# Kernel optimization log

Measured on AMD Instinct MI355X. Metric: run time of the kernel, lower is better.

Reference implementation:

```python
import jax, jax.numpy as jnp
import numpy as np

T, B, I, H = 512, 64, 300, 1000


def setup_inputs() -> dict:
    key = jax.random.key(0)
    k_in, k_wih, k_whh = jax.random.split(key, 3)
    s_ih = 1.0 / np.sqrt(H)
    return {
        "inputs": jax.random.normal(k_in, (T, B, I), dtype=jnp.float32),
        "h0": jnp.zeros((B, H), dtype=jnp.float32),
        "c0": jnp.zeros((B, H), dtype=jnp.float32),
        "W_ih": jax.random.normal(k_wih, (4 * H, I), dtype=jnp.float32) * s_ih,
        "W_hh": jax.random.normal(k_whh, (4 * H, H), dtype=jnp.float32) * s_ih,
        "b_ih": jnp.zeros((4 * H,), dtype=jnp.float32),
        "b_hh": jnp.zeros((4 * H,), dtype=jnp.float32),
    }


def reference(inputs, h0, c0, W_ih, W_hh, b_ih, b_hh):
    # Precompute input projections for all timesteps in one big GEMM:
    # [T,B,I] @ [I,4H] -> [T,B,4H]
    x_gates = jnp.einsum('tbi,gi->tbg', inputs, W_ih) + b_ih + b_hh

    def step(carry, xg):
        h, c = carry
        gates = xg + h @ W_hh.T            # [B, 4H]
        i, f, g, o = jnp.split(gates, 4, axis=-1)  # PyTorch gate order i,f,g,o
        i = jax.nn.sigmoid(i)
        f = jax.nn.sigmoid(f)
        g = jnp.tanh(g)
        o = jax.nn.sigmoid(o)
        c_new = f * c + i * g
        h_new = o * jnp.tanh(c_new)
        return (h_new, c_new), h_new

    (_, _), outputs = jax.lax.scan(step, (h0, c0), x_gates)
    return outputs  # [T, B, H] — stacked per-timestep outputs
```

## Files before the change

### kernel.cpp

```cpp
#include <hip/hip_runtime.h>

#define Tn 512
#define Bn 64
#define In 300
#define Hn 1000
#define G4H 4000
#define KP 1024
#define KI 320
#define NB 125

typedef __attribute__((ext_vector_type(8))) short bf16x8;
typedef __attribute__((ext_vector_type(4))) float f32x4;
typedef unsigned int u32;
typedef unsigned short u16;
typedef unsigned long long u64;

__device__ __forceinline__ u16 f2bf(float x) {
  union { float f; u32 u; } v; v.f = x;
  u32 r = (v.u + 0x7fffu + ((v.u >> 16) & 1u)) >> 16;
  return (u16)r;
}
__device__ __forceinline__ float bf2f(u16 s) {
  union { u32 u; float f; } v; v.u = ((u32)s) << 16;
  return v.f;
}
__device__ __forceinline__ float sigm(float x) { return 1.f / (1.f + __expf(-x)); }
__device__ __forceinline__ float tanh_f(float x) {
  float e = __expf(2.f * x);
  return 1.f - 2.f / (e + 1.f);
}

__device__ __forceinline__ u64 aload64(const u64* p) {
  return __hip_atomic_load((u64*)p, __ATOMIC_RELAXED, __HIP_MEMORY_SCOPE_AGENT);
}
__device__ __forceinline__ void astore64(u64* p, u64 v) {
  __hip_atomic_store(p, v, __ATOMIC_RELAXED, __HIP_MEMORY_SCOPE_AGENT);
}
__device__ __forceinline__ u32 aload32(const u32* p) {
  return __hip_atomic_load((u32*)p, __ATOMIC_RELAXED, __HIP_MEMORY_SCOPE_AGENT);
}
__device__ __forceinline__ void astore32(u32* p, u32 v) {
  __hip_atomic_store(p, v, __ATOMIC_RELAXED, __HIP_MEMORY_SCOPE_AGENT);
}

__global__ void conv_pad(const float* __restrict__ src, u16* __restrict__ dst,
                         int rows, int scols, int dcols) {
  int idx = blockIdx.x * 256 + threadIdx.x;
  int total = rows * dcols;
  if (idx >= total) return;
  int r = idx / dcols, k = idx - r * dcols;
  float v = (k < scols) ? src[(size_t)r * scols + k] : 0.f;
  dst[idx] = f2bf(v);
}

__global__ void init_scan(const float* __restrict__ h0, u16* __restrict__ ring,
                          u32* __restrict__ bar) {
  int idx = blockIdx.x * 256 + threadIdx.x;
  if (idx < 4096) bar[idx] = 0;
  if (idx < Bn * KP) {
    int b = idx >> 10, k = idx & (KP - 1);
    float v = (k < Hn) ? h0[b * Hn + k] : 0.f;
    ring[idx] = f2bf(v);
  }
  for (int i = idx; i < (Tn - 1) * Bn * 24; i += 512 * 256) {
    int slot = 1 + i / (Bn * 24);
    int rem = i % (Bn * 24);
    int row = rem / 24, col = 1000 + (rem % 24);
    ring[(size_t)slot * (Bn * KP) + (size_t)row * KP + col] = 0;
  }
}

template<bool XF32>
__global__ void __launch_bounds__(256)
gemm_xg(const u16* __restrict__ A, const u16* __restrict__ Wb,
        const float* __restrict__ b_ih, const float* __restrict__ b_hh,
        void* __restrict__ xg_out) {
  const int lane = threadIdx.x & 63, w = threadIdx.x >> 6;
  const int m0 = blockIdx.x * 64, n0 = blockIdx.y * 64;
  f32x4 acc[4] = {};
  const int arow = m0 + w * 16 + (lane & 15);
  const int koff = (lane >> 4) * 8;
  int nrow[4];
#pragma unroll
  for (int nt = 0; nt < 4; ++nt) {
    int n = n0 + nt * 16 + (lane & 15);
    nrow[nt] = (n < G4H) ? n : (G4H - 1);
  }
  for (int kc = 0; kc < KI / 32; ++kc) {
    bf16x8 a = *(const bf16x8*)(A + (size_t)arow * KI + kc * 32 + koff);
#pragma unroll
    for (int nt = 0; nt < 4; ++nt) {
      bf16x8 bb = *(const bf16x8*)(Wb + (size_t)nrow[nt] * KI + kc * 32 + koff);
      acc[nt] = __builtin_amdgcn_mfma_f32_16x16x32_bf16(a, bb, acc[nt], 0, 0, 0);
    }
  }
#pragma unroll
  for (int nt = 0; nt < 4; ++nt) {
    int col = n0 + nt * 16 + (lane & 15);
    if (col >= G4H) continue;
    float bias = b_ih[col] + b_hh[col];
    u32 g = (u32)col / 1000u;
    int j = col - (int)g * 1000;
    int nb8 = j >> 3, cc = j & 7;
    int slot = ((int)g << 3) | cc;
    int mrow = m0 + w * 16 + (lane >> 4) * 4;
#pragma unroll
    for (int r = 0; r < 4; ++r) {
      int m = mrow + r;
      int t = m >> 6, b = m & 63;
      float v = acc[nt][r] + bias;
      size_t o = (((size_t)t * NB + nb8) * 64 + b) * 32 + slot;
      if constexpr (XF32) ((float*)xg_out)[o] = v;
      else                ((u16*)xg_out)[o] = f2bf(v);
    }
  }
}

template<bool XF32>
__global__ void __launch_bounds__(256, 1)
lstm_scan(const float* __restrict__ Whh, const float* __restrict__ c0,
          const void* __restrict__ xg_, u16* __restrict__ ring,
          float* __restrict__ out, u32* __restrict__ bar) {
  __shared__ float Sc[4][16][33];
  __shared__ __align__(8) u16 hs[64][8];
  __shared__ int lready[4];
  const int tid = threadIdx.x;
  const int lane = tid & 63;
  const int w = tid >> 6;
  const int nb = blockIdx.x;
  const int s = lane & 15;
  const int q = lane >> 4;

  if (tid < 4) lready[tid] = 0;

  u32* flags = bar + 256;
  u64* ring64 = (u64*)ring;

  bf16x8 wreg0[32], wreg1[32];
  {
    const int jj0 = s;
    const float* wrow0 =
        Whh + (size_t)((jj0 >> 3) * Hn + nb * 8 + (jj0 & 7)) * Hn;
    const int jj1 = 16 + s;
    const float* wrow1 =
        Whh + (size_t)((jj1 >> 3) * Hn + nb * 8 + (jj1 & 7)) * Hn;
#pragma unroll
    for (int kc = 0; kc < 32; ++kc) {
      const int k0 = kc * 32 + q * 8;
      bf16x8 v0, v1;
#pragma unroll
      for (int j = 0; j < 8; ++j) {
        float f0 = (k0 + j < Hn) ? wrow0[k0 + j] : 0.f;
        float f1 = (k0 + j < Hn) ? wrow1[k0 + j] : 0.f;
        v0[j] = (short)f2bf(f0);
        v1[j] = (short)f2bf(f1);
      }
      wreg0[kc] = v0;
      wreg1[kc] = v1;
    }
  }

  const int bl = lane >> 3, cc = lane & 7;
  const int jh = nb * 8 + cc;
  float cst[2];
  cst[0] = c0[(size_t)(w * 16 + bl) * Hn + jh];
  cst[1] = c0[(size_t)(w * 16 + bl + 8) * Hn + jh];

  const float* xf = (const float*)xg_;
  const u16* xh = (const u16*)xg_;

  float xa[8];
  {
    size_t base = (((size_t)0 * NB + nb) * 64 + w * 16 + q * 4) * 32 + s;
#pragma unroll
    for (int nt = 0; nt < 2; ++nt)
#pragma unroll
      for (int r = 0; r < 4; ++r) {
        size_t o = base + (size_t)r * 32 + nt * 16;
        xa[nt * 4 + r] = XF32 ? xf[o] : bf2f(xh[o]);
      }
  }

  int pidx = 32 * w + (lane & 31);
  if (pidx >= NB) pidx = NB - 1;
  const u32* pf = flags + (size_t)pidx * 16;

  __syncthreads();

  for (int t = 0; t < Tn; ++t) {
    const u16* hrow = ring + (size_t)t * (Bn * KP) +
                      (size_t)(w * 16 + s) * KP + q * 8;
    u64* hn = ring64 + (size_t)(t + 1) * (Bn * KP / 4);

    if (t > 0) {
      while (true) {
        u32 f = (lane < 32) ? aload32(pf) : 0xffffffffu;
        if (__all((int)(f >= (u32)t))) break;
        __builtin_amdgcn_s_sleep(1);
      }
      if (lane == 0)
        __hip_atomic_store(&lready[w], t, __ATOMIC_RELAXED,
                           __HIP_MEMORY_SCOPE_WORKGROUP);
    }

    auto wait_g = [&](int g) {
      if (g == w) return;
      while (__hip_atomic_load(&lready[g], __ATOMIC_RELAXED,
                               __HIP_MEMORY_SCOPE_WORKGROUP) < t) {
      }
      __builtin_amdgcn_sched_barrier(0);
    };
    auto load8 = [&](bf16x8* buf, int kcb) {
#pragma unroll
      for (int k = 0; k < 8; ++k)
        buf[k] = *(const bf16x8*)(hrow + (size_t)(kcb + k) * 32);
    };

    f32x4 a00 = {xa[0], xa[1], xa[2], xa[3]};
    f32x4 a01 = {0.f, 0.f, 0.f, 0.f};
    f32x4 a10 = {xa[4], xa[5], xa[6], xa[7]};
    f32x4 a11 = {0.f, 0.f, 0.f, 0.f};

    bf16x8 b0[8], b1[8];
    wait_g(0);
    load8(b0, 0);
    wait_g(1);
    load8(b1, 8);
#pragma unroll
    for (int k = 0; k < 8; ++k) {
      a00 = __builtin_amdgcn_mfma_f32_16x16x32_bf16(b0[k], wreg0[k], a00, 0, 0, 0);
      a10 = __builtin_amdgcn_mfma_f32_16x16x32_bf16(b0[k], wreg1[k], a10, 0, 0, 0);
    }
    wait_g(2);
    load8(b0, 16);
#pragma unroll
    for (int k = 0; k < 8; ++k) {
      a00 = __builtin_amdgcn_mfma_f32_16x16x32_bf16(b1[k], wreg0[8 + k], a00, 0, 0, 0);
      a10 = __builtin_amdgcn_mfma_f32_16x16x32_bf16(b1[k], wreg1[8 + k], a10, 0, 0, 0);
    }
    wait_g(3);
    load8(b1, 24);
#pragma unroll
    for (int k = 0; k < 8; ++k) {
      a01 = __builtin_amdgcn_mfma_f32_16x16x32_bf16(b0[k], wreg0[16 + k], a01, 0, 0, 0);
      a11 = __builtin_amdgcn_mfma_f32_16x16x32_bf16(b0[k], wreg1[16 + k], a11, 0, 0, 0);
    }
#pragma unroll
    for (int k = 0; k < 8; ++k) {
      a01 = __builtin_amdgcn_mfma_f32_16x16x32_bf16(b1[k], wreg0[24 + k], a01, 0, 0, 0);
      a11 = __builtin_amdgcn_mfma_f32_16x16x32_bf16(b1[k], wreg1[24 + k], a11, 0, 0, 0);
    }

#pragma unroll
    for (int r = 0; r < 4; ++r) {
      Sc[w][q * 4 + r][s]      = a00[r] + a01[r];
      Sc[w][q * 4 + r][16 + s] = a10[r] + a11[r];
    }

    float hv[2];
#pragma unroll
    for (int k = 0; k < 2; ++k) {
      int bb = bl + 8 * k;
      float gi = Sc[w][bb][cc];
      float gf = Sc[w][bb][8 + cc];
      float gg = Sc[w][bb][16 + cc];
      float go = Sc[w][bb][24 + cc];
      float iv = sigm(gi), fv = sigm(gf), gv = tanh_f(gg), ov = sigm(go);
      cst[k] = fv * cst[k] + iv * gv;
      hv[k] = ov * tanh_f(cst[k]);
      out[((size_t)t * Bn + (w * 16 + bb)) * Hn + jh] = hv[k];
      hs[w * 16 + bb][cc] = f2bf(hv[k]);
    }

    if (t != Tn - 1) {
      __syncthreads();
      if (tid < 128) {
        int row = tid >> 1, half = tid & 1;
        u64 hvv = *(const u64*)&hs[row][half * 4];
        u64* ad = hn + (size_t)row * 256 + nb * 2 + half;
        astore64(ad, hvv);
        __builtin_amdgcn_s_sleep(2);
        while (aload64(ad) != hvv) __builtin_amdgcn_s_sleep(1);
      }
      __syncthreads();
      if (tid == 0) astore32(flags + (size_t)nb * 16, (u32)(t + 1));

      {
        size_t base =
            (((size_t)(t + 1) * NB + nb) * 64 + w * 16 + q * 4) * 32 + s;
#pragma unroll
        for (int nt = 0; nt < 2; ++nt)
#pragma unroll
          for (int r = 0; r < 4; ++r) {
            size_t o = base + (size_t)r * 32 + nt * 16;
            xa[nt * 4 + r] = XF32 ? xf[o] : bf2f(xh[o]);
          }
      }
    }
  }
}

extern "C" void kernel_launch(void* const* d_in, const int* in_sizes, int n_in,
                              void* d_out, int out_size, void* d_ws, size_t ws_size,
                              hipStream_t stream) {
  const float* inputs = (const float*)d_in[0];
  const float* h0 = (const float*)d_in[1];
  const float* c0 = (const float*)d_in[2];
  const float* W_ih = (const float*)d_in[3];
  const float* W_hh = (const float*)d_in[4];
  const float* b_ih = (const float*)d_in[5];
  const float* b_hh = (const float*)d_in[6];
  float* out = (float*)d_out;

  char* ws = (char*)d_ws;
  size_t off = 0;
  auto carve = [&](size_t bytes) {
    char* p = ws + off;
    off = (off + bytes + 255) & ~(size_t)255;
    return p;
  };
  u32* bar = (u32*)carve(16384);
  u16* in_bf = (u16*)carve((size_t)Tn * Bn * KI * 2);
  u16* wih_bf = (u16*)carve((size_t)G4H * KI * 2);
  u16* ring = (u16*)carve((size_t)Tn * Bn * KP * 2);
  size_t fixed = off;
  size_t xg_f32 = (size_t)Tn * NB * 64 * 32 * 4;
  bool xf32 = (ws_size >= fixed + xg_f32);
  void* xg = (void*)carve(xf32 ? xg_f32 : xg_f32 / 2);

  int tot_in = Tn * Bn * KI;
  conv_pad<<<dim3((tot_in + 255) / 256), dim3(256), 0, stream>>>(
      inputs, in_bf, Tn * Bn, In, KI);
  int tot_w = G4H * KI;
  conv_pad<<<dim3((tot_w + 255) / 256), dim3(256), 0, stream>>>(
      W_ih, wih_bf, G4H, In, KI);
  init_scan<<<dim3(512), dim3(256), 0, stream>>>(h0, ring, bar);

  if (xf32) {
    gemm_xg<true><<<dim3(Tn * Bn / 64, (G4H + 63) / 64), dim3(256), 0, stream>>>(
        in_bf, wih_bf, b_ih, b_hh, xg);
    lstm_scan<true><<<dim3(NB), dim3(256), 0, stream>>>(
        W_hh, c0, xg, ring, out, bar);
  } else {
    gemm_xg<false><<<dim3(Tn * Bn / 64, (G4H + 63) / 64), dim3(256), 0, stream>>>(
        in_bf, wih_bf, b_ih, b_hh, xg);
    lstm_scan<false><<<dim3(NB), dim3(256), 0, stream>>>(
        W_hh, c0, xg, ring, out, bar);
  }
}
```

Measured before the change: 4.091 ms.

## Replace per-block barrier with per-wave flags in persistent LSTM scan

Each wave now publishes its own batch-slice h rows and sets a per-(block,wave) flag, so the two __syncthreads and the LDS lready handshake per timestep are removed. Consumer waves poll only the 125 flags for their own batch rows (four loads per lane) rather than one flag per block. This decouples waves so they can proceed independently, but it multiplies flag traffic by four and makes every lane poll, which may add memory contention during the spin.

Measured after the change: 6.253 ms. +52.8%, slower.

```diff
diff --git a/kernel.cpp b/kernel.cpp
--- a/kernel.cpp
+++ b/kernel.cpp
@@ -56,7 +56,7 @@
 __global__ void init_scan(const float* __restrict__ h0, u16* __restrict__ ring,
                           u32* __restrict__ bar) {
   int idx = blockIdx.x * 256 + threadIdx.x;
-  if (idx < 4096) bar[idx] = 0;
+  if (idx < 16384) bar[idx] = 0;
   if (idx < Bn * KP) {
     int b = idx >> 10, k = idx & (KP - 1);
     float v = (k < Hn) ? h0[b * Hn + k] : 0.f;
@@ -122,16 +122,13 @@
           const void* __restrict__ xg_, u16* __restrict__ ring,
           float* __restrict__ out, u32* __restrict__ bar) {
   __shared__ float Sc[4][16][33];
-  __shared__ __align__(8) u16 hs[64][8];
-  __shared__ int lready[4];
+  __shared__ __align__(8) u16 hs[4][16][8];
   const int tid = threadIdx.x;
   const int lane = tid & 63;
   const int w = tid >> 6;
   const int nb = blockIdx.x;
   const int s = lane & 15;
   const int q = lane >> 4;
-
-  if (tid < 4) lready[tid] = 0;
 
   u32* flags = bar + 256;
   u64* ring64 = (u64*)ring;
@@ -181,11 +178,13 @@
       }
   }
 
-  int pidx = 32 * w + (lane & 31);
-  if (pidx >= NB) pidx = NB - 1;
-  const u32* pf = flags + (size_t)pidx * 16;
-
-  __syncthreads();
+  const u32* pf[4];
+#pragma unroll
+  for (int j = 0; j < 4; ++j) {
+    int idx = lane + 32 * j;
+    if (idx > NB - 1) idx = NB - 1;
+    pf[j] = flags + ((size_t)idx * 4 + w) * 16;
+  }
 
   for (int t = 0; t < Tn; ++t) {
     const u16* hrow = ring + (size_t)t * (Bn * KP) +
@@ -194,22 +193,17 @@
 
     if (t > 0) {
       while (true) {
-        u32 f = (lane < 32) ? aload32(pf) : 0xffffffffu;
-        if (__all((int)(f >= (u32)t))) break;
+        u32 f0 = aload32(pf[0]);
+        u32 f1 = aload32(pf[1]);
+        u32 f2 = aload32(pf[2]);
+        u32 f3 = aload32(pf[3]);
+        int ok = (f0 >= (u32)t) & (f1 >= (u32)t) &
+                 (f2 >= (u32)t) & (f3 >= (u32)t);
+        if (__all(ok)) break;
         __builtin_amdgcn_s_sleep(1);
       }
-      if (lane == 0)
-        __hip_atomic_store(&lready[w], t, __ATOMIC_RELAXED,
-                           __HIP_MEMORY_SCOPE_WORKGROUP);
-    }
-
-    auto wait_g = [&](int g) {
-      if (g == w) return;
-      while (__hip_atomic_load(&lready[g], __ATOMIC_RELAXED,
-                               __HIP_MEMORY_SCOPE_WORKGROUP) < t) {
-      }
-      __builtin_amdgcn_sched_barrier(0);
-    };
+    }
+
     auto load8 = [&](bf16x8* buf, int kcb) {
 #pragma unroll
       for (int k = 0; k < 8; ++k)
@@ -222,23 +216,19 @@
     f32x4 a11 = {0.f, 0.f, 0.f, 0.f};
 
     bf16x8 b0[8], b1[8];
-    wait_g(0);
     load8(b0, 0);
-    wait_g(1);
     load8(b1, 8);
 #pragma unroll
     for (int k = 0; k < 8; ++k) {
       a00 = __builtin_amdgcn_mfma_f32_16x16x32_bf16(b0[k], wreg0[k], a00, 0, 0, 0);
       a10 = __builtin_amdgcn_mfma_f32_16x16x32_bf16(b0[k], wreg1[k], a10, 0, 0, 0);
     }
-    wait_g(2);
     load8(b0, 16);
 #pragma unroll
     for (int k = 0; k < 8; ++k) {
       a00 = __builtin_amdgcn_mfma_f32_16x16x32_bf16(b1[k], wreg0[8 + k], a00, 0, 0, 0);
       a10 = __builtin_amdgcn_mfma_f32_16x16x32_bf16(b1[k], wreg1[8 + k], a10, 0, 0, 0);
     }
-    wait_g(3);
     load8(b1, 24);
 #pragma unroll
     for (int k = 0; k < 8; ++k) {
@@ -269,21 +259,21 @@
       cst[k] = fv * cst[k] + iv * gv;
       hv[k] = ov * tanh_f(cst[k]);
       out[((size_t)t * Bn + (w * 16 + bb)) * Hn + jh] = hv[k];
-      hs[w * 16 + bb][cc] = f2bf(hv[k]);
+      hs[w][bb][cc] = f2bf(hv[k]);
     }
 
     if (t != Tn - 1) {
-      __syncthreads();
-      if (tid < 128) {
-        int row = tid >> 1, half = tid & 1;
-        u64 hvv = *(const u64*)&hs[row][half * 4];
-        u64* ad = hn + (size_t)row * 256 + nb * 2 + half;
+      asm volatile("s_waitcnt lgkmcnt(0)" ::: "memory");
+      if (lane < 32) {
+        int row = lane >> 1, half = lane & 1;
+        u64 hvv = *(const u64*)&hs[w][row][half * 4];
+        u64* ad = hn + (size_t)(w * 16 + row) * 256 + nb * 2 + half;
         astore64(ad, hvv);
         __builtin_amdgcn_s_sleep(2);
         while (aload64(ad) != hvv) __builtin_amdgcn_s_sleep(1);
       }
-      __syncthreads();
-      if (tid == 0) astore32(flags + (size_t)nb * 16, (u32)(t + 1));
+      if (lane == 0)
+        astore32(flags + ((size_t)nb * 4 + w) * 16, (u32)(t + 1));
 
       {
         size_t base =
@@ -319,7 +309,7 @@
     off = (off + bytes + 255) & ~(size_t)255;
     return p;
   };
-  u32* bar = (u32*)carve(16384);
+  u32* bar = (u32*)carve(65536);
   u16* in_bf = (u16*)carve((size_t)Tn * Bn * KI * 2);
   u16* wih_bf = (u16*)carve((size_t)G4H * KI * 2);
   u16* ring = (u16*)carve((size_t)Tn * Bn * KP * 2);
```
